# Optimization experiments

Measured on AMD Instinct MI355X. Metric: run time of the kernel, lower is better.

## Reference

```python
import jax, jax.numpy as jnp
import numpy as np

B, S, H = 8, 2048, 1024


def setup_inputs() -> dict:
    key = jax.random.key(0)
    ks = jax.random.split(key, 12)
    s = 1.0 / np.sqrt(H)
    return {
        "_q": jax.random.normal(ks[0], (B, S, H), jnp.float32),
        "_kv": jax.random.normal(ks[1], (B, S, H), jnp.float32),
        "W_kv": jax.random.normal(ks[2], (H, 2 * H), jnp.float32) * s,
        "b_kv": jnp.zeros((2 * H,), jnp.float32),
        "W_q": jax.random.normal(ks[3], (H, H), jnp.float32) * s,
        "b_q": jnp.zeros((H,), jnp.float32),
        "W1": jax.random.normal(ks[4], (H, 4 * H), jnp.float32) * s,
        "b1": jnp.zeros((4 * H,), jnp.float32),
        "W2": jax.random.normal(ks[5], (4 * H, H), jnp.float32) * (1.0 / np.sqrt(4 * H)),
        "b2": jnp.zeros((H,), jnp.float32),
    }


def reference(_q, _kv, W_kv, b_kv, W_q, b_q, W1, b1, W2, b2):
    # kv projection then split into k, v: [B,S,H] each
    kv = _kv @ W_kv + b_kv
    k, v = jnp.split(kv, 2, axis=-1)
    q = _q @ W_q + b_q
    # NOTE: original module does single-head attention with NO 1/sqrt(d) scale
    scores = jnp.einsum('bqh,bkh->bqk', q, k)          # [B,Sq,Sk]
    attn = jax.nn.softmax(scores, axis=-1)
    out = jnp.einsum('bqk,bkh->bqh', attn, v)          # [B,Sq,H]
    # MLP: Linear -> exact GELU -> (Dropout=identity in eval) -> Linear
    hidden = jax.nn.gelu(out @ W1 + b1, approximate=False)
    return hidden @ W2 + b2
```

## Files before the change

### kernel.cpp

```cpp
#include <hip/hip_runtime.h>
#include <hip/hip_bf16.h>

typedef __attribute__((ext_vector_type(8))) short short8;
typedef __attribute__((ext_vector_type(8))) _Float16 half8;
typedef __attribute__((ext_vector_type(4))) _Float16 half4v;
typedef __attribute__((ext_vector_type(4))) float f32x4;
typedef unsigned short us;

#define GLDS16(G, L) __builtin_amdgcn_global_load_lds( \
    (const __attribute__((address_space(1))) void*)(G), \
    (__attribute__((address_space(3))) void*)(L), 16, 0, 0)

__global__ void k_sentinel(float* p) {
    if (threadIdx.x == 0 && blockIdx.x == 0) p[0] = 12345.0f;
}

__global__ void k_cast(const float* __restrict__ in, _Float16* __restrict__ out, long n4) {
    long i = (long)blockIdx.x * blockDim.x + threadIdx.x;
    long stride = (long)gridDim.x * blockDim.x;
    for (; i < n4; i += stride) {
        float4 v = ((const float4*)in)[i];
        half4v h;
        h[0] = (_Float16)v.x; h[1] = (_Float16)v.y;
        h[2] = (_Float16)v.z; h[3] = (_Float16)v.w;
        ((half4v*)out)[i] = h;
    }
}

__global__ void k_wtransh(const float* __restrict__ in, _Float16* __restrict__ out,
                          int K, int N) {
    __shared__ float tile[32][33];
    int n0 = blockIdx.x * 32, k0 = blockIdx.y * 32;
    int tx = threadIdx.x, ty = threadIdx.y;
#pragma unroll
    for (int r = ty; r < 32; r += 8)
        tile[r][tx] = in[(size_t)(k0 + r) * N + n0 + tx];
    __syncthreads();
#pragma unroll
    for (int r = ty; r < 32; r += 8)
        out[(size_t)(n0 + r) * K + k0 + tx] = (_Float16)tile[tx][r];
}

__device__ __forceinline__ float wredmax(float v) {
#pragma unroll
    for (int off = 32; off > 0; off >>= 1) v = fmaxf(v, __shfl_xor(v, off, 64));
    return v;
}
__device__ __forceinline__ float wredsum(float v) {
#pragma unroll
    for (int off = 32; off > 0; off >>= 1) v += __shfl_xor(v, off, 64);
    return v;
}

__global__ __launch_bounds__(256) void k_softmax(const float* __restrict__ S,
                                                 _Float16* __restrict__ P) {
    __shared__ float red[8];
    size_t base = (size_t)blockIdx.x * 2048;
    int t = threadIdx.x;
    float4 a = ((const float4*)(S + base))[2 * t];
    float4 b = ((const float4*)(S + base))[2 * t + 1];
    float v[8] = {a.x, a.y, a.z, a.w, b.x, b.y, b.z, b.w};
    float m = v[0];
#pragma unroll
    for (int j = 1; j < 8; j++) m = fmaxf(m, v[j]);
    m = wredmax(m);
    int wv = t >> 6;
    if ((t & 63) == 0) red[wv] = m;
    __syncthreads();
    m = fmaxf(fmaxf(red[0], red[1]), fmaxf(red[2], red[3]));
    float s = 0.f;
#pragma unroll
    for (int j = 0; j < 8; j++) { v[j] = __expf(v[j] - m); s += v[j]; }
    s = wredsum(s);
    if ((t & 63) == 0) red[4 + wv] = s;
    __syncthreads();
    s = red[4] + red[5] + red[6] + red[7];
    float inv = 1.f / s;
    half4v o0, o1;
#pragma unroll
    for (int j = 0; j < 4; j++) o0[j] = (_Float16)(v[j] * inv);
#pragma unroll
    for (int j = 0; j < 4; j++) o1[j] = (_Float16)(v[4 + j] * inv);
    ((half4v*)(P + base))[2 * t] = o0;
    ((half4v*)(P + base))[2 * t + 1] = o1;
}

template <int OUT_MODE, bool GELU_ACT>
__global__ __launch_bounds__(256, 2) void k_gemmh(
    const us* __restrict__ A, const us* __restrict__ B,
    const float* __restrict__ bias, void* __restrict__ C,
    int N, int K, long sA, long sB, long sC) {
    __shared__ __align__(16) us lds[2][4096];

    const int tid = threadIdx.x;
    const int wave = tid >> 6, lane = tid & 63;
    const int wr = wave >> 1, wc = wave & 1;
    const int l15 = lane & 15, l4 = lane >> 4;
    const int m0 = blockIdx.x * 128, n0 = blockIdx.y * 128;
    const us* pA = A + (size_t)blockIdx.z * sA;
    const us* pB = B + (size_t)blockIdx.z * sB;
    const size_t zC = (size_t)blockIdx.z * sC;

    f32x4 acc[4][4] = {};

    auto stage = [&](const us* __restrict__ g, us* l, int r0, int kk) {
#pragma unroll
        for (int i = 0; i < 2; i++) {
            int s = (i << 8) + tid;
            int row = s >> 2;
            int chunk = (s & 3) ^ ((row >> 1) & 3);
            const us* src = g + (size_t)(r0 + row) * K + kk + chunk * 8;
            us* dst = l + (((i << 8) + (wave << 6)) << 3);
            GLDS16(src, dst);
        }
    };

    for (int kk = 0; kk < K; kk += 32) {
        stage(pA, lds[0], m0, kk);
        stage(pB, lds[1], n0, kk);
        __syncthreads();

        short8 af[4], bf[4];
#pragma unroll
        for (int f = 0; f < 4; f++) {
            int ra = (wr << 6) + (f << 4) + l15;
            af[f] = *(const short8*)(&lds[0][(ra << 5) + ((l4 ^ ((ra >> 1) & 3)) << 3)]);
            int rb = (wc << 6) + (f << 4) + l15;
            bf[f] = *(const short8*)(&lds[1][(rb << 5) + ((l4 ^ ((rb >> 1) & 3)) << 3)]);
        }
#pragma unroll
        for (int fm = 0; fm < 4; fm++)
#pragma unroll
            for (int fn = 0; fn < 4; fn++)
                acc[fm][fn] = __builtin_amdgcn_mfma_f32_16x16x32_f16(
                    __builtin_bit_cast(half8, af[fm]), __builtin_bit_cast(half8, bf[fn]),
                    acc[fm][fn], 0, 0, 0);
        __syncthreads();
    }

    float bv[4];
#pragma unroll
    for (int fn = 0; fn < 4; fn++)
        bv[fn] = bias ? bias[n0 + (wc << 6) + (fn << 4) + l15] : 0.f;

#pragma unroll
    for (int fm = 0; fm < 4; fm++) {
        int rbase = m0 + (wr << 6) + (fm << 4) + (l4 << 2);
#pragma unroll
        for (int fn = 0; fn < 4; fn++) {
            int col = n0 + (wc << 6) + (fn << 4) + l15;
#pragma unroll
            for (int r = 0; r < 4; r++) {
                float x = acc[fm][fn][r] + bv[fn];
                if (GELU_ACT) x = 0.5f * x * (1.f + erff(x * 0.70710678118654752f));
                size_t row = (size_t)(rbase + r);
                if (OUT_MODE == 5) {
                    size_t o = ((row >> 11) * (size_t)N + (size_t)col) * 2048 + (row & 2047);
                    ((_Float16*)C)[o] = (_Float16)x;
                } else {
                    size_t o = zC + row * N + col;
                    if (OUT_MODE == 0) ((float*)C)[o] = x;
                    else               ((_Float16*)C)[o] = (_Float16)x;
                }
            }
        }
    }
}

extern "C" void kernel_launch(void* const* d_in, const int* in_sizes, int n_in,
                              void* d_out, int out_size, void* d_ws, size_t ws_size,
                              hipStream_t stream) {
    (void)in_sizes; (void)n_in; (void)out_size;
    const float* g_q   = (const float*)d_in[0];
    const float* g_kv  = (const float*)d_in[1];
    const float* g_Wkv = (const float*)d_in[2];
    const float* g_bkv = (const float*)d_in[3];
    const float* g_Wq  = (const float*)d_in[4];
    const float* g_bq  = (const float*)d_in[5];
    const float* g_W1  = (const float*)d_in[6];
    const float* g_b1  = (const float*)d_in[7];
    const float* g_W2  = (const float*)d_in[8];
    const float* g_b2  = (const float*)d_in[9];

    const size_t MiB = 1048576ull;
    const long SH = 2048L * 1024;
    const long SS = 2048L * 2048;
    char* ws = (char*)d_ws;
    dim3 tb32(32, 8);

    if (ws_size < 176 * MiB) {
        k_sentinel<<<1, 64, 0, stream>>>((float*)d_out);
        return;
    }

    _Float16* xq  = (_Float16*)ws;
    char*     REGION = ws + 32 * MiB;
    _Float16* kf    = (_Float16*)REGION;
    _Float16* vT    = (_Float16*)(REGION + 32 * MiB);
    _Float16* P_all = (_Float16*)(REGION + 64 * MiB);
    _Float16* hidden = (_Float16*)REGION;
    char* wreg = ws + 160 * MiB;
    _Float16* WkvT = (_Float16*)wreg;
    _Float16* WqT  = (_Float16*)(wreg + 4 * MiB);
    _Float16* W1T  = (_Float16*)wreg;
    _Float16* W2T  = (_Float16*)(wreg + 8 * MiB);

    _Float16* xkv      = (_Float16*)d_out;
    float*    scores_c = (float*)d_out;
    _Float16* q_all    = (_Float16*)((char*)d_out + 32 * MiB);

    k_wtransh<<<dim3(64, 32), tb32, 0, stream>>>(g_Wkv, WkvT, 1024, 2048);
    k_wtransh<<<dim3(32, 32), tb32, 0, stream>>>(g_Wq, WqT, 1024, 1024);
    k_cast<<<4096, 256, 0, stream>>>(g_kv, xkv, 4194304);
    k_cast<<<4096, 256, 0, stream>>>(g_q, xq, 4194304);

    k_gemmh<4, false><<<dim3(128, 8, 1), 256, 0, stream>>>(
        (const us*)xkv, (const us*)WkvT, g_bkv, kf, 1024, 1024, 0, 0, 0);
    k_gemmh<5, false><<<dim3(128, 8, 1), 256, 0, stream>>>(
        (const us*)xkv, (const us*)(WkvT + (size_t)1024 * 1024), g_bkv + 1024, vT,
        1024, 1024, 0, 0, 0);
    k_gemmh<4, false><<<dim3(128, 8, 1), 256, 0, stream>>>(
        (const us*)xq, (const us*)WqT, g_bq, q_all, 1024, 1024, 0, 0, 0);

    for (int c = 0; c < 4; ++c) {
        size_t ro = (size_t)c * 4096 * 1024;
        k_gemmh<0, false><<<dim3(16, 16, 2), 256, 0, stream>>>(
            (const us*)(q_all + ro), (const us*)(kf + ro), nullptr, scores_c,
            2048, 1024, SH, SH, SS);
        k_softmax<<<4096, 256, 0, stream>>>(scores_c, P_all + (size_t)c * 2 * SS);
    }

    k_gemmh<4, false><<<dim3(16, 8, 8), 256, 0, stream>>>(
        (const us*)P_all, (const us*)vT, nullptr, xq, 1024, 2048, SS, SH, SH);

    k_wtransh<<<dim3(128, 32), tb32, 0, stream>>>(g_W1, W1T, 1024, 4096);
    k_wtransh<<<dim3(32, 128), tb32, 0, stream>>>(g_W2, W2T, 4096, 1024);
    k_gemmh<4, true><<<dim3(128, 32, 1), 256, 0, stream>>>(
        (const us*)xq, (const us*)W1T, g_b1, hidden, 4096, 1024, 0, 0, 0);
    k_gemmh<0, false><<<dim3(128, 8, 1), 256, 0, stream>>>(
        (const us*)hidden, (const us*)W2T, g_b2, d_out, 1024, 4096, 0, 0, 0);
}
```

Measured before the change: 817.6 us.

## Deepen GEMM K-tile to 64 with 8-way XOR swizzle and XCD-aware block remap

The GEMM kernel now stages a 64-wide K slice per iteration (twice the LDS per buffer) with an 8-chunk XOR swizzle. It issues two MFMA sub-steps per barrier pair, halving the number of synchronisations and loop overheads. It also remaps workgroup IDs so consecutive tiles land on the same XCD to improve L2 reuse. The cost is 32KB of LDS per block, which may limit occupancy, and the remap assumes the tile count divides evenly by 8.

```diff
diff --git a/kernel.cpp b/kernel.cpp
--- a/kernel.cpp
+++ b/kernel.cpp
@@ -86,17 +86,24 @@
 }
 
 template <int OUT_MODE, bool GELU_ACT>
-__global__ __launch_bounds__(256, 2) void k_gemmh(
+__global__ __launch_bounds__(256, 2) void k_gemm64(
     const us* __restrict__ A, const us* __restrict__ B,
     const float* __restrict__ bias, void* __restrict__ C,
     int N, int K, long sA, long sB, long sC) {
-    __shared__ __align__(16) us lds[2][4096];
+    __shared__ __align__(16) us ldsA[8192];
+    __shared__ __align__(16) us ldsB[8192];
 
     const int tid = threadIdx.x;
     const int wave = tid >> 6, lane = tid & 63;
     const int wr = wave >> 1, wc = wave & 1;
     const int l15 = lane & 15, l4 = lane >> 4;
-    const int m0 = blockIdx.x * 128, n0 = blockIdx.y * 128;
+
+    const int gx = gridDim.x;
+    const int nwg = gx * gridDim.y;
+    const int lid = blockIdx.x + gx * blockIdx.y;
+    const int wg = (lid & 7) * (nwg >> 3) + (lid >> 3);
+    const int m0 = (wg % gx) * 128, n0 = (wg / gx) * 128;
+
     const us* pA = A + (size_t)blockIdx.z * sA;
     const us* pB = B + (size_t)blockIdx.z * sB;
     const size_t zC = (size_t)blockIdx.z * sC;
@@ -105,36 +112,41 @@
 
     auto stage = [&](const us* __restrict__ g, us* l, int r0, int kk) {
 #pragma unroll
-        for (int i = 0; i < 2; i++) {
+        for (int i = 0; i < 4; i++) {
             int s = (i << 8) + tid;
-            int row = s >> 2;
-            int chunk = (s & 3) ^ ((row >> 1) & 3);
-            const us* src = g + (size_t)(r0 + row) * K + kk + chunk * 8;
+            int row = s >> 3;
+            int cl = (s & 7) ^ (row & 7);
+            const us* src = g + (size_t)(r0 + row) * K + kk + (cl << 3);
             us* dst = l + (((i << 8) + (wave << 6)) << 3);
             GLDS16(src, dst);
         }
     };
 
-    for (int kk = 0; kk < K; kk += 32) {
-        stage(pA, lds[0], m0, kk);
-        stage(pB, lds[1], n0, kk);
+    for (int kk = 0; kk < K; kk += 64) {
+        stage(pA, ldsA, m0, kk);
+        stage(pB, ldsB, n0, kk);
         __syncthreads();
 
-        short8 af[4], bf[4];
-#pragma unroll
-        for (int f = 0; f < 4; f++) {
-            int ra = (wr << 6) + (f << 4) + l15;
-            af[f] = *(const short8*)(&lds[0][(ra << 5) + ((l4 ^ ((ra >> 1) & 3)) << 3)]);
-            int rb = (wc << 6) + (f << 4) + l15;
-            bf[f] = *(const short8*)(&lds[1][(rb << 5) + ((l4 ^ ((rb >> 1) & 3)) << 3)]);
+#pragma unroll
+        for (int ks = 0; ks < 2; ks++) {
+            short8 af[4], bf[4];
+#pragma unroll
+            for (int f = 0; f < 4; f++) {
+                int ra = (wr << 6) + (f << 4) + l15;
+                af[f] = *(const short8*)(
+                    &ldsA[(ra << 6) + ((((ks << 2) | l4) ^ (ra & 7)) << 3)]);
+                int rb = (wc << 6) + (f << 4) + l15;
+                bf[f] = *(const short8*)(
+                    &ldsB[(rb << 6) + ((((ks << 2) | l4) ^ (rb & 7)) << 3)]);
+            }
+#pragma unroll
+            for (int fm = 0; fm < 4; fm++)
+#pragma unroll
+                for (int fn = 0; fn < 4; fn++)
+                    acc[fm][fn] = __builtin_amdgcn_mfma_f32_16x16x32_f16(
+                        __builtin_bit_cast(half8, af[fm]), __builtin_bit_cast(half8, bf[fn]),
+                        acc[fm][fn], 0, 0, 0);
         }
-#pragma unroll
-        for (int fm = 0; fm < 4; fm++)
-#pragma unroll
-            for (int fn = 0; fn < 4; fn++)
-                acc[fm][fn] = __builtin_amdgcn_mfma_f32_16x16x32_f16(
-                    __builtin_bit_cast(half8, af[fm]), __builtin_bit_cast(half8, bf[fn]),
-                    acc[fm][fn], 0, 0, 0);
         __syncthreads();
     }
 
@@ -214,29 +226,29 @@
     k_cast<<<4096, 256, 0, stream>>>(g_kv, xkv, 4194304);
     k_cast<<<4096, 256, 0, stream>>>(g_q, xq, 4194304);
 
-    k_gemmh<4, false><<<dim3(128, 8, 1), 256, 0, stream>>>(
+    k_gemm64<4, false><<<dim3(128, 8, 1), 256, 0, stream>>>(
         (const us*)xkv, (const us*)WkvT, g_bkv, kf, 1024, 1024, 0, 0, 0);
-    k_gemmh<5, false><<<dim3(128, 8, 1), 256, 0, stream>>>(
+    k_gemm64<5, false><<<dim3(128, 8, 1), 256, 0, stream>>>(
         (const us*)xkv, (const us*)(WkvT + (size_t)1024 * 1024), g_bkv + 1024, vT,
         1024, 1024, 0, 0, 0);
-    k_gemmh<4, false><<<dim3(128, 8, 1), 256, 0, stream>>>(
+    k_gemm64<4, false><<<dim3(128, 8, 1), 256, 0, stream>>>(
         (const us*)xq, (const us*)WqT, g_bq, q_all, 1024, 1024, 0, 0, 0);
 
     for (int c = 0; c < 4; ++c) {
         size_t ro = (size_t)c * 4096 * 1024;
-        k_gemmh<0, false><<<dim3(16, 16, 2), 256, 0, stream>>>(
+        k_gemm64<0, false><<<dim3(16, 16, 2), 256, 0, stream>>>(
             (const us*)(q_all + ro), (const us*)(kf + ro), nullptr, scores_c,
             2048, 1024, SH, SH, SS);
         k_softmax<<<4096, 256, 0, stream>>>(scores_c, P_all + (size_t)c * 2 * SS);
     }
 
-    k_gemmh<4, false><<<dim3(16, 8, 8), 256, 0, stream>>>(
+    k_gemm64<4, false><<<dim3(16, 8, 8), 256, 0, stream>>>(
         (const us*)P_all, (const us*)vT, nullptr, xq, 1024, 2048, SS, SH, SH);
 
     k_wtransh<<<dim3(128, 32), tb32, 0, stream>>>(g_W1, W1T, 1024, 4096);
     k_wtransh<<<dim3(32, 128), tb32, 0, stream>>>(g_W2, W2T, 4096, 1024);
-    k_gemmh<4, true><<<dim3(128, 32, 1), 256, 0, stream>>>(
+    k_gemm64<4, true><<<dim3(128, 32, 1), 256, 0, stream>>>(
         (const us*)xq, (const us*)W1T, g_b1, hidden, 4096, 1024, 0, 0, 0);
-    k_gemmh<0, false><<<dim3(128, 8, 1), 256, 0, stream>>>(
+    k_gemm64<0, false><<<dim3(128, 8, 1), 256, 0, stream>>>(
         (const us*)hidden, (const us*)W2T, g_b2, d_out, 1024, 4096, 0, 0, 0);
 }
```

New measurement: 827.0 us. About the same (+1.1%).

## Double-buffer GEMM LDS tiles with prefetch and use polynomial erf in GELU

Applied to the files above, without the earlier changes.

The GEMM kernel now keeps two LDS buffers. It issues the global-to-LDS loads for the next K tile before computing on the current one, so memory latency overlaps with MFMA work, and it drops one barrier per iteration. It also raises wave priority around the MFMA block and replaces erff in the GELU epilogue with an Abramowitz-Stegun polynomial approximation. LDS use doubles to 32KB per block, which can limit occupancy. The erf approximation has an error of about 1e-7 and stays within fp16 output precision.

```diff
diff --git a/kernel.cpp b/kernel.cpp
--- a/kernel.cpp
+++ b/kernel.cpp
@@ -13,6 +13,18 @@
 
 __global__ void k_sentinel(float* p) {
     if (threadIdx.x == 0 && blockIdx.x == 0) p[0] = 12345.0f;
+}
+
+__device__ __forceinline__ float fast_gelu(float x) {
+    float ax = fabsf(x) * 0.70710678118654752f;
+    float t = __frcp_rn(fmaf(0.3275911f, ax, 1.0f));
+    float p = fmaf(1.061405429f, t, -1.453152027f);
+    p = fmaf(p, t, 1.421413741f);
+    p = fmaf(p, t, -0.284496736f);
+    p = fmaf(p, t, 0.254829592f);
+    p = p * t * __expf(-ax * ax);
+    float erfv = __builtin_copysignf(1.0f - p, x);
+    return 0.5f * x * (1.0f + erfv);
 }
 
 __global__ void k_cast(const float* __restrict__ in, _Float16* __restrict__ out, long n4) {
@@ -86,17 +98,18 @@
 }
 
 template <int OUT_MODE, bool GELU_ACT>
-__global__ __launch_bounds__(256, 2) void k_gemmh(
+__global__ __launch_bounds__(256, 2) void k_gemm2p(
     const us* __restrict__ A, const us* __restrict__ B,
     const float* __restrict__ bias, void* __restrict__ C,
     int N, int K, long sA, long sB, long sC) {
-    __shared__ __align__(16) us lds[2][4096];
+    __shared__ __align__(16) us lds[2][2][4096];
 
     const int tid = threadIdx.x;
     const int wave = tid >> 6, lane = tid & 63;
     const int wr = wave >> 1, wc = wave & 1;
     const int l15 = lane & 15, l4 = lane >> 4;
     const int m0 = blockIdx.x * 128, n0 = blockIdx.y * 128;
+
     const us* pA = A + (size_t)blockIdx.z * sA;
     const us* pB = B + (size_t)blockIdx.z * sB;
     const size_t zC = (size_t)blockIdx.z * sC;
@@ -115,19 +128,27 @@
         }
     };
 
+    stage(pA, &lds[0][0][0], m0, 0);
+    stage(pB, &lds[0][1][0], n0, 0);
+    __syncthreads();
+
     for (int kk = 0; kk < K; kk += 32) {
-        stage(pA, lds[0], m0, kk);
-        stage(pB, lds[1], n0, kk);
-        __syncthreads();
+        const int cur = (kk >> 5) & 1;
+        if (kk + 32 < K) {
+            stage(pA, &lds[cur ^ 1][0][0], m0, kk + 32);
+            stage(pB, &lds[cur ^ 1][1][0], n0, kk + 32);
+        }
+        __builtin_amdgcn_sched_barrier(0);
 
         short8 af[4], bf[4];
 #pragma unroll
         for (int f = 0; f < 4; f++) {
             int ra = (wr << 6) + (f << 4) + l15;
-            af[f] = *(const short8*)(&lds[0][(ra << 5) + ((l4 ^ ((ra >> 1) & 3)) << 3)]);
+            af[f] = *(const short8*)(&lds[cur][0][(ra << 5) + ((l4 ^ ((ra >> 1) & 3)) << 3)]);
             int rb = (wc << 6) + (f << 4) + l15;
-            bf[f] = *(const short8*)(&lds[1][(rb << 5) + ((l4 ^ ((rb >> 1) & 3)) << 3)]);
-        }
+            bf[f] = *(const short8*)(&lds[cur][1][(rb << 5) + ((l4 ^ ((rb >> 1) & 3)) << 3)]);
+        }
+        __builtin_amdgcn_s_setprio(1);
 #pragma unroll
         for (int fm = 0; fm < 4; fm++)
 #pragma unroll
@@ -135,6 +156,7 @@
                 acc[fm][fn] = __builtin_amdgcn_mfma_f32_16x16x32_f16(
                     __builtin_bit_cast(half8, af[fm]), __builtin_bit_cast(half8, bf[fn]),
                     acc[fm][fn], 0, 0, 0);
+        __builtin_amdgcn_s_setprio(0);
         __syncthreads();
     }
 
@@ -152,7 +174,7 @@
 #pragma unroll
             for (int r = 0; r < 4; r++) {
                 float x = acc[fm][fn][r] + bv[fn];
-                if (GELU_ACT) x = 0.5f * x * (1.f + erff(x * 0.70710678118654752f));
+                if (GELU_ACT) x = fast_gelu(x);
                 size_t row = (size_t)(rbase + r);
                 if (OUT_MODE == 5) {
                     size_t o = ((row >> 11) * (size_t)N + (size_t)col) * 2048 + (row & 2047);
@@ -214,29 +236,29 @@
     k_cast<<<4096, 256, 0, stream>>>(g_kv, xkv, 4194304);
     k_cast<<<4096, 256, 0, stream>>>(g_q, xq, 4194304);
 
-    k_gemmh<4, false><<<dim3(128, 8, 1), 256, 0, stream>>>(
+    k_gemm2p<4, false><<<dim3(128, 8, 1), 256, 0, stream>>>(
         (const us*)xkv, (const us*)WkvT, g_bkv, kf, 1024, 1024, 0, 0, 0);
-    k_gemmh<5, false><<<dim3(128, 8, 1), 256, 0, stream>>>(
+    k_gemm2p<5, false><<<dim3(128, 8, 1), 256, 0, stream>>>(
         (const us*)xkv, (const us*)(WkvT + (size_t)1024 * 1024), g_bkv + 1024, vT,
         1024, 1024, 0, 0, 0);
-    k_gemmh<4, false><<<dim3(128, 8, 1), 256, 0, stream>>>(
+    k_gemm2p<4, false><<<dim3(128, 8, 1), 256, 0, stream>>>(
         (const us*)xq, (const us*)WqT, g_bq, q_all, 1024, 1024, 0, 0, 0);
 
     for (int c = 0; c < 4; ++c) {
         size_t ro = (size_t)c * 4096 * 1024;
-        k_gemmh<0, false><<<dim3(16, 16, 2), 256, 0, stream>>>(
+        k_gemm2p<0, false><<<dim3(16, 16, 2), 256, 0, stream>>>(
             (const us*)(q_all + ro), (const us*)(kf + ro), nullptr, scores_c,
             2048, 1024, SH, SH, SS);
         k_softmax<<<4096, 256, 0, stream>>>(scores_c, P_all + (size_t)c * 2 * SS);
     }
 
-    k_gemmh<4, false><<<dim3(16, 8, 8), 256, 0, stream>>>(
+    k_gemm2p<4, false><<<dim3(16, 8, 8), 256, 0, stream>>>(
         (const us*)P_all, (const us*)vT, nullptr, xq, 1024, 2048, SS, SH, SH);
 
     k_wtransh<<<dim3(128, 32), tb32, 0, stream>>>(g_W1, W1T, 1024, 4096);
     k_wtransh<<<dim3(32, 128), tb32, 0, stream>>>(g_W2, W2T, 4096, 1024);
-    k_gemmh<4, true><<<dim3(128, 32, 1), 256, 0, stream>>>(
+    k_gemm2p<4, true><<<dim3(128, 32, 1), 256, 0, stream>>>(
         (const us*)xq, (const us*)W1T, g_b1, hidden, 4096, 1024, 0, 0, 0);
-    k_gemmh<0, false><<<dim3(128, 8, 1), 256, 0, stream>>>(
+    k_gemm2p<0, false><<<dim3(128, 8, 1), 256, 0, stream>>>(
         (const us*)hidden, (const us*)W2T, g_b2, d_out, 1024, 4096, 0, 0, 0);
 }
```

New measurement: 818.3 us. Within noise of the previous version (+0.1%).
